# Optimization experiments

Hardware: AMD Instinct MI355X
Metric: run time of the kernel (lower is better)

Reference implementation:

```python
import jax, jax.numpy as jnp
import numpy as np

S, V, T = 128, 64, 128
N_RBF, CUTOFF = 16, 6.0
N_ATOM, N_PROT, N_FRAG, N_BATCH = 8192, 16384, 1024, 8
K, R, EPS = 32, 3.0, 1e-4
ES_DIM = N_RBF + S + S + T  # 400
HID = 256
GATE = S + 2 * V  # 256


def rbf_encode(d):
    mu = jnp.linspace(0.0, CUTOFF, N_RBF)
    gamma = N_RBF / CUTOFF
    return jnp.exp(-jnp.square(gamma * (d[..., None] - mu)))


def tp_conv(hs, hv, src, dst, diff, es, valid, n_dst, W1, b1, W2, b2, Ws, Wv):
    """Gather -> edge-scalar-gated tensor product -> scatter-add (EquivariantTPConv)."""
    w = jax.nn.silu(es @ W1 + b1) @ W2 + b2                      # [E, S+2V] edge gates
    unit = diff / (jnp.linalg.norm(diff, axis=-1, keepdims=True) + 1e-8)
    xs = hs[src] @ Ws                                            # [E, S]
    xv = jnp.einsum('evc,vw->ewc', hv[src], Wv)                  # [E, V, 3]
    ms = jnp.where(valid[:, None], w[:, :S] * xs, 0.0)
    mv = jnp.where(valid[:, None, None],
                   w[:, S:S + V, None] * xv + w[:, S + V:, None] * unit[:, None, :], 0.0)
    agg_s = jax.ops.segment_sum(ms, dst, num_segments=n_dst)
    agg_v = jax.ops.segment_sum(mv.reshape(-1, V * 3), dst, num_segments=n_dst).reshape(n_dst, V, 3)
    return agg_s, agg_v


def fragment_inertia(local_pos, fragment_id):
    r2 = jnp.sum(local_pos * local_pos, axis=-1)
    eye = jnp.eye(3, dtype=local_pos.dtype)
    I_atom = r2[:, None, None] * eye - local_pos[:, :, None] * local_pos[:, None, :]
    I_frag = jax.ops.segment_sum(I_atom.reshape(-1, 9), fragment_id, num_segments=N_FRAG).reshape(N_FRAG, 3, 3)
    trace = jnp.trace(I_frag, axis1=-2, axis2=-1)[:, None, None]
    return I_frag + EPS * jnp.maximum(trace, 1.0) * eye


def _forward(atom_pos, prot_pos, local_pos, h_atom_s, h_atom_v, h_prot_s, h_prot_v,
             h_frag_s, h_frag_v, t_emb_atom,
             W1_ra, b1_ra, W2_ra, b2_ra, Ws_ra, Wv_ra,
             W1_af, b1_af, W2_af, b2_af, Ws_af, Wv_af,
             Wo_s, Wo_v, Wf_s, Wf_v,
             fragment_id, atom_batch, prot_batch):
    # ---- bipartite radius graph prot -> atom via masked cdist + topk ----
    d2 = (jnp.sum(atom_pos * atom_pos, -1)[:, None]
          + jnp.sum(prot_pos * prot_pos, -1)[None, :]
          - 2.0 * atom_pos @ prot_pos.T)
    dist = jnp.sqrt(jnp.maximum(d2, 0.0))                        # [N_ATOM, N_PROT]
    mask = (dist <= R) & (atom_batch[:, None] == prot_batch[None, :])
    dinf = jnp.where(mask, dist, jnp.inf)
    neg_top, src = jax.lax.top_k(-dinf, K)                       # K nearest per atom
    valid = jnp.isfinite(neg_top).reshape(-1)
    src = src.reshape(-1)
    dst = jnp.repeat(jnp.arange(N_ATOM), K)
    # ---- residue->atom TP conv ----
    diff_ra = atom_pos[dst] - prot_pos[src]
    dist_ra = jnp.linalg.norm(diff_ra, axis=-1)
    ra_es = jnp.concatenate([rbf_encode(dist_ra), h_prot_s[src], h_atom_s[dst], t_emb_atom[dst]], -1)
    ms, mv = tp_conv(h_prot_s, h_prot_v, src, dst, diff_ra, ra_es, valid, N_ATOM,
                     W1_ra, b1_ra, W2_ra, b2_ra, Ws_ra, Wv_ra)
    ha_s = h_atom_s + jax.nn.silu(ms @ Wo_s)
    ha_v = h_atom_v + jnp.einsum('nvc,vw->nwc', mv, Wo_v)
    # ---- fragment centers + atom->frag re-lift TP conv ----
    ones = jnp.ones((N_ATOM,), atom_pos.dtype)
    cnt = jnp.maximum(jax.ops.segment_sum(ones, fragment_id, num_segments=N_FRAG), 1.0)
    T_frag = jax.ops.segment_sum(atom_pos, fragment_id, num_segments=N_FRAG) / cnt[:, None]
    r_af = atom_pos - T_frag[fragment_id]
    af_es = jnp.concatenate([rbf_encode(jnp.linalg.norm(r_af, axis=-1)), ha_s,
                             h_frag_s[fragment_id], t_emb_atom], -1)
    af_valid = jnp.ones((N_ATOM,), bool)
    fs, fv = tp_conv(ha_s, ha_v, jnp.arange(N_ATOM), fragment_id, r_af, af_es, af_valid, N_FRAG,
                     W1_af, b1_af, W2_af, b2_af, Ws_af, Wv_af)
    hf_s = h_frag_s + jax.nn.silu(fs @ Wf_s)
    hf_v = h_frag_v + jnp.einsum('nvc,vw->nwc', fv, Wf_v)
    I_frag = fragment_inertia(local_pos, fragment_id)
    # single packed output [N_ATOM, 2*(S+3V)+9]; frag quantities gathered per atom
    return jnp.concatenate([ha_s, ha_v.reshape(N_ATOM, -1),
                            hf_s[fragment_id], hf_v.reshape(N_FRAG, -1)[fragment_id],
                            I_frag.reshape(N_FRAG, 9)[fragment_id]], -1)


def setup_inputs() -> dict:
    key = jax.random.key(0)
    ks = jax.random.split(key, 32)
    def w(k, shape, fan_in):
        return jax.random.normal(k, shape, jnp.float32) / np.sqrt(fan_in).astype(np.float32)
    return dict(
        atom_pos=jax.random.normal(ks[0], (N_ATOM, 3), jnp.float32),
        prot_pos=jax.random.normal(ks[1], (N_PROT, 3), jnp.float32),
        local_pos=jax.random.normal(ks[2], (N_ATOM, 3), jnp.float32),
        h_atom_s=jax.random.normal(ks[3], (N_ATOM, S), jnp.float32),
        h_atom_v=jax.random.normal(ks[4], (N_ATOM, V, 3), jnp.float32),
        h_prot_s=jax.random.normal(ks[5], (N_PROT, S), jnp.float32),
        h_prot_v=jax.random.normal(ks[6], (N_PROT, V, 3), jnp.float32),
        h_frag_s=jax.random.normal(ks[7], (N_FRAG, S), jnp.float32),
        h_frag_v=jax.random.normal(ks[8], (N_FRAG, V, 3), jnp.float32),
        t_emb_atom=jax.random.normal(ks[9], (N_ATOM, T), jnp.float32),
        W1_ra=w(ks[10], (ES_DIM, HID), ES_DIM), b1_ra=jnp.zeros((HID,), jnp.float32),
        W2_ra=w(ks[11], (HID, GATE), HID), b2_ra=jnp.zeros((GATE,), jnp.float32),
        Ws_ra=w(ks[12], (S, S), S), Wv_ra=w(ks[13], (V, V), V),
        W1_af=w(ks[14], (ES_DIM, HID), ES_DIM), b1_af=jnp.zeros((HID,), jnp.float32),
        W2_af=w(ks[15], (HID, GATE), HID), b2_af=jnp.zeros((GATE,), jnp.float32),
        Ws_af=w(ks[16], (S, S), S), Wv_af=w(ks[17], (V, V), V),
        Wo_s=w(ks[18], (S, S), S), Wo_v=w(ks[19], (V, V), V),
        Wf_s=w(ks[20], (S, S), S), Wf_v=w(ks[21], (V, V), V),
        fragment_id=jax.random.randint(ks[22], (N_ATOM,), 0, N_FRAG),
        atom_batch=jnp.sort(jax.random.randint(ks[23], (N_ATOM,), 0, N_BATCH)),
        prot_batch=jnp.sort(jax.random.randint(ks[24], (N_PROT,), 0, N_BATCH)),
    )


def reference(atom_pos, prot_pos, local_pos, h_atom_s, h_atom_v, h_prot_s, h_prot_v,
              h_frag_s, h_frag_v, t_emb_atom,
              W1_ra, b1_ra, W2_ra, b2_ra, Ws_ra, Wv_ra,
              W1_af, b1_af, W2_af, b2_af, Ws_af, Wv_af,
              Wo_s, Wo_v, Wf_s, Wf_v,
              fragment_id, atom_batch, prot_batch):
    return _forward(atom_pos, prot_pos, local_pos, h_atom_s, h_atom_v, h_prot_s, h_prot_v,
                    h_frag_s, h_frag_v, t_emb_atom,
                    W1_ra, b1_ra, W2_ra, b2_ra, Ws_ra, Wv_ra,
                    W1_af, b1_af, W2_af, b2_af, Ws_af, Wv_af,
                    Wo_s, Wo_v, Wf_s, Wf_v,
                    fragment_id, atom_batch, prot_batch)
```

## Files before the change

kernel.cpp:

```cpp
#include <hip/hip_runtime.h>
#include <hip/hip_bf16.h>

#define N_ATOM 8192
#define N_PROT 16384
#define N_FRAG 1024
#define KNN    32
#define OUTC   649

typedef __attribute__((ext_vector_type(8))) short bf16x8;
typedef __attribute__((ext_vector_type(4))) float f32x4;

__device__ __forceinline__ float silu_f(float x){ return x / (1.f + __expf(-x)); }
__device__ __forceinline__ unsigned long long ullmin2(unsigned long long a, unsigned long long b){ return a < b ? a : b; }

__device__ __forceinline__ short f2bf(float x){
    __hip_bfloat16 h = __float2bfloat16(x);
    return *reinterpret_cast<short*>(&h);
}
__device__ __forceinline__ unsigned f2bf2(float lo, float hi){
    __hip_bfloat162 h2;
    h2.x = __float2bfloat16(lo);
    h2.y = __float2bfloat16(hi);
    return *reinterpret_cast<unsigned*>(&h2);
}
__device__ __forceinline__ float bf2f(short s){
    return __uint_as_float(((unsigned)(unsigned short)s) << 16);
}

__global__ void k_ranges(const int* __restrict__ pbatch, int* __restrict__ pstart){
    int b = threadIdx.x;
    if (b <= 8){
        int lo = 0, hi = N_PROT;
        while (lo < hi){ int mid = (lo + hi) >> 1; if (pbatch[mid] < b) lo = mid + 1; else hi = mid; }
        pstart[b] = lo;
    }
}

__global__ __launch_bounds__(256) void k_cvt(const float* __restrict__ hps,
                                             const float* __restrict__ hpv,
                                             short* __restrict__ hpsB,
                                             short* __restrict__ hpvT){
    int id = blockIdx.x*256 + threadIdx.x;
    if (id < N_PROT*16){
        const float* s = hps + (size_t)id*8;
        float4 x0 = *(const float4*)(s);
        float4 x1 = *(const float4*)(s+4);
        unsigned* d = (unsigned*)(hpsB + (size_t)id*8);
        d[0] = f2bf2(x0.x, x0.y); d[1] = f2bf2(x0.z, x0.w);
        d[2] = f2bf2(x1.x, x1.y); d[3] = f2bf2(x1.z, x1.w);
    } else {
        int id2 = id - N_PROT*16;
        if (id2 < N_PROT*24){
            int j = id2 / 24, r = id2 % 24;
            short tmp[8];
#pragma unroll
            for (int u = 0; u < 8; ++u){
                int o = r*8 + u, c = o >> 6, v = o & 63;
                tmp[u] = f2bf(hpv[(size_t)j*192 + v*3 + c]);
            }
            *(bf16x8*)(hpvT + (size_t)j*192 + r*8) = *(bf16x8*)tmp;
        }
    }
}

__global__ __launch_bounds__(256) void k_knn(const float* __restrict__ apos,
                                             const float* __restrict__ ppos,
                                             const int* __restrict__ abatch,
                                             const int* __restrict__ pstart,
                                             int* __restrict__ src_out){
    __shared__ int h1[256];
    __shared__ int s_info[4];
    __shared__ int s_nsel;
    __shared__ int s_nbound;
    __shared__ unsigned long long s_bound[512];

    const int i = blockIdx.x, t = threadIdx.x;
    const int lane = t & 63;
    const int b = abatch[i];
    const int p0 = pstart[b], p1 = pstart[b+1];
    const float ax = apos[i*3+0], ay = apos[i*3+1], az = apos[i*3+2];
    const float a2 = ax*ax + ay*ay + az*az;
    const float BINSCALE = 256.0f / 9.0f;

    unsigned kb[12];
    int jj[12];
    int bn[12];
#pragma unroll
    for (int q = 0; q < 12; ++q){
        int j = p0 + q*256 + t;
        unsigned kk = 0xFFFFFFFFu;
        int bin = -1;
        if (j < p1){
            float px = ppos[j*3+0], py = ppos[j*3+1], pz = ppos[j*3+2];
            float p2 = px*px + py*py + pz*pz;
            float dt = ax*px + ay*py + az*pz;
            float d2 = fmaxf((a2 + p2) - 2.0f*dt, 0.f);
            if (d2 <= 9.0f){
                kk = __float_as_uint(d2);
                bin = (int)(d2 * BINSCALE);
                if (bin > 255) bin = 255;
            }
        }
        kb[q] = kk; jj[q] = j; bn[q] = bin;
    }
    h1[t] = 0;
    if (t == 0){ s_nsel = 0; s_nbound = 0; }
    __syncthreads();
#pragma unroll
    for (int q = 0; q < 12; ++q)
        if (bn[q] >= 0) atomicAdd(&h1[bn[q]], 1);
    __syncthreads();
    if (t < 64){
        int base = t*4;
// ... 2 lines not shown
        int sc = lsum;
#pragma unroll
        for (int off = 1; off < 64; off <<= 1){
            int v = __shfl_up(sc, off);
            if (lane >= off) sc += v;
        }
        int ex = sc - lsum;
        h1[base]   = ex + a0;
        h1[base+1] = ex + a0 + a1;
        h1[base+2] = ex + a0 + a1 + a2i;
        h1[base+3] = sc;
        if (t == 63) s_info[3] = sc;
    }
    __syncthreads();
    const int total = s_info[3];
    const int kth = (total < KNN) ? total : KNN;
    if (kth > 0){
        int cum  = h1[t];
        int prev = (t == 0) ? 0 : h1[t-1];
        if (cum >= kth && prev < kth){ s_info[0] = t; }
    }
    __syncthreads();
    const int B = s_info[0];
    if (kth > 0){
#pragma unroll
        for (int q = 0; q < 12; ++q){
            if (bn[q] < 0) continue;
            if (bn[q] < B){
                int pos = atomicAdd(&s_nsel, 1);
                src_out[i*KNN + pos] = jj[q];
            } else if (bn[q] == B){
                int bi = atomicAdd(&s_nbound, 1);
                if (bi < 512) s_bound[bi] = ((unsigned long long)kb[q] << 32) | (unsigned)jj[q];
            }
        }
    }
    __syncthreads();
    const int base_n = s_nsel;
    const int R = kth - base_n;
    if (t < 64 && R > 0){
        int L = s_nbound; if (L > 512) L = 512;
        for (int r = 0; r < R; ++r){
            unsigned long long m = ~0ull;
            for (int idx = lane; idx < L; idx += 64) m = ullmin2(m, s_bound[idx]);
#pragma unroll
            for (int off = 32; off >= 1; off >>= 1)
                m = ullmin2(m, (unsigned long long)__shfl_xor((unsigned long long)m, off));
            if (lane == 0) src_out[i*KNN + base_n + r] = (int)(unsigned)(m & 0xFFFFFFFFull);
            for (int idx = lane; idx < L; idx += 64)
                if (s_bound[idx] == m) s_bound[idx] = ~0ull;
        }
    }
    if (t < KNN && t >= kth) src_out[i*KNN + t] = -1;
}

__global__ void k_fragsum(const float* __restrict__ apos, const float* __restrict__ lpos,
                          const int* __restrict__ fid,
                          float* __restrict__ cnt, float* __restrict__ tsum, float* __restrict__ isum){
    int a = blockIdx.x*256 + threadIdx.x;
    if (a >= N_ATOM) return;
    int f = fid[a];
    atomicAdd(&cnt[f], 1.f);
    atomicAdd(&tsum[f*3+0], apos[a*3+0]);
    atomicAdd(&tsum[f*3+1], apos[a*3+1]);
    atomicAdd(&tsum[f*3+2], apos[a*3+2]);
    float x = lpos[a*3+0], y = lpos[a*3+1], z = lpos[a*3+2];
    float r2 = x*x + y*y + z*z;
    atomicAdd(&isum[f*9+0], r2 - x*x);
    atomicAdd(&isum[f*9+1], -(x*y));
    atomicAdd(&isum[f*9+2], -(x*z));
    atomicAdd(&isum[f*9+3], -(y*x));
    atomicAdd(&isum[f*9+4], r2 - y*y);
    atomicAdd(&isum[f*9+5], -(y*z));
    atomicAdd(&isum[f*9+6], -(z*x));
    atomicAdd(&isum[f*9+7], -(z*y));
    atomicAdd(&isum[f*9+8], r2 - z*z);
}

__global__ __launch_bounds__(1024) void k_csr_prefix(const float* __restrict__ cnt,
                                                     const float* __restrict__ tsum,
                                                     const float* __restrict__ isum,
                                                     int* __restrict__ csr_off,
                                                     int* __restrict__ csr_cur,
                                                     float* __restrict__ tfrag,
                                                     float* __restrict__ ifin){
    __shared__ int s[1024];
    int t = threadIdx.x;
    float cn_raw = cnt[t];
    int v = (int)cn_raw;
    s[t] = v;
    {
        float cn = fmaxf(cn_raw, 1.f);
        tfrag[t*3+0] = tsum[t*3+0] / cn;
        tfrag[t*3+1] = tsum[t*3+1] / cn;
        tfrag[t*3+2] = tsum[t*3+2] / cn;
        float tr  = isum[t*9+0] + isum[t*9+4] + isum[t*9+8];
        float add = 1e-4f * fmaxf(tr, 1.f);
#pragma unroll
        for (int q = 0; q < 9; ++q){
            float vv = isum[t*9+q];
            if (q == 0 || q == 4 || q == 8) vv += add;
            ifin[t*9+q] = vv;
        }
    }
    __syncthreads();
    for (int off = 1; off < 1024; off <<= 1){
        int x = (t >= off) ? s[t-off] : 0;
        __syncthreads();
        s[t] += x;
        __syncthreads();
    }
    int incl = s[t];
    int excl = incl - v;
    csr_off[t] = excl;
    csr_cur[t] = excl;
    if (t == 1023) csr_off[1024] = incl;
}

__global__ void k_csr_scatter(const int* __restrict__ fid, int* __restrict__ csr_cur,
                              int* __restrict__ csr_atom){
    int a = blockIdx.x*256 + threadIdx.x;
    if (a >= N_ATOM) return;
    int f = fid[a];
    int pos = atomicAdd(&csr_cur[f], 1);
    csr_atom[pos] = a;
}

__global__ void k_pack(const float* __restrict__ W1, const float* __restrict__ W2,
                       const float* __restrict__ Ws, const float* __restrict__ Wv,
                       const float* __restrict__ W1a, const float* __restrict__ W2a,
                       const float* __restrict__ Wsa, const float* __restrict__ Wva,
                       const float* __restrict__ Wos, const float* __restrict__ Wov,
                       short* __restrict__ W1p, short* __restrict__ W2p,
                       short* __restrict__ Wsp, short* __restrict__ Wvp,
                       short* __restrict__ W1cp,
                       short* __restrict__ W1ap, short* __restrict__ W2ap,
                       short* __restrict__ Wsap, short* __restrict__ Wvap,
                       short* __restrict__ Wosp, short* __restrict__ Wovp){
    int id = blockIdx.x*256 + threadIdx.x;
    if (id < 5120){
        int kt = id/1024, rem = id%1024, nt = rem/64, l = rem%64;
#pragma unroll
        for (int jj = 0; jj < 8; ++jj){
            int k = kt*32 + ((l>>4)<<3) + jj, n = nt*16 + (l&15);
            W1p[(size_t)id*8 + jj] = (k < 144) ? f2bf(W1[(size_t)k*256 + n]) : (short)0;
        }
    } else if (id < 13312){
        int id2 = id - 5120;
        int kt = id2/1024, rem = id2%1024, nt = rem/64, l = rem%64;
#pragma unroll
        for (int jj = 0; jj < 8; ++jj){
            int k = kt*32 + ((l>>4)<<3) + jj, n = nt*16 + (l&15);
            W2p[(size_t)id2*8 + jj] = f2bf(W2[(size_t)k*256 + n]);
        }
    } else if (id < 15360){
        int id2 = id - 13312;
        int kt = id2/512, rem = id2%512, nt = rem/64, l = rem%64;
#pragma unroll
        for (int jj = 0; jj < 8; ++jj){
            int k = kt*32 + ((l>>4)<<3) + jj, n = nt*16 + (l&15);
            Wsp[(size_t)id2*8 + jj] = f2bf(Ws[(size_t)k*128 + n]);
        }
    } else if (id < 15872){
        int id2 = id - 15360;
        int kt = id2/256, rem = id2%256, nt = rem/64, l = rem%64;
#pragma unroll
        for (int jj = 0; jj < 8; ++jj){
            int k = kt*32 + ((l>>4)<<3) + jj, n = nt*16 + (l&15);
            Wvp[(size_t)id2*8 + jj] = f2bf(Wv[(size_t)k*64 + n]);
        }
    } else if (id < 24064){
        int id2 = id - 15872;
        int kt = id2/1024, rem = id2%1024, nt = rem/64, l = rem%64;
#pragma unroll
        for (int jj = 0; jj < 8; ++jj){
            int k = kt*32 + ((l>>4)<<3) + jj, n = nt*16 + (l&15);
            W1cp[(size_t)id2*8 + jj] = f2bf(W1[(size_t)(144 + k)*256 + n]);
        }
    } else if (id < 37376){
        int id2 = id - 24064;
        int kt = id2/1024, rem = id2%1024, nt = rem/64, l = rem%64;
#pragma unroll
        for (int jj = 0; jj < 8; ++jj){
            int k = kt*32 + ((l>>4)<<3) + jj, n = nt*16 + (l&15);
            W1ap[(size_t)id2*8 + jj] = (k < 400) ? f2bf(W1a[(size_t)k*256 + n]) : (short)0;
        }
    } else if (id < 45568){
        int id2 = id - 37376;
        int kt = id2/1024, rem = id2%1024, nt = rem/64, l = rem%64;
#pragma unroll
        for (int jj = 0; jj < 8; ++jj){
            int k = kt*32 + ((l>>4)<<3) + jj, n = nt*16 + (l&15);
            W2ap[(size_t)id2*8 + jj] = f2bf(W2a[(size_t)k*256 + n]);
        }
    } else if (id < 47616){
        int id2 = id - 45568;
        int kt = id2/512, rem = id2%512, nt = rem/64, l = rem%64;
#pragma unroll
        for (int jj = 0; jj < 8; ++jj){
            int k = kt*32 + ((l>>4)<<3) + jj, n = nt*16 + (l&15);
            Wsap[(size_t)id2*8 + jj] = f2bf(Wsa[(size_t)k*128 + n]);
        }
    } else if (id < 48128){
        int id2 = id - 47616;
        int kt = id2/256, rem = id2%256, nt = rem/64, l = rem%64;
#pragma unroll
        for (int jj = 0; jj < 8; ++jj){
            int k = kt*32 + ((l>>4)<<3) + jj, n = nt*16 + (l&15);
            Wvap[(size_t)id2*8 + jj] = f2bf(Wva[(size_t)k*64 + n]);
        }
    } else if (id < 50176){
        int id2 = id - 48128;
        int kt = id2/512, rem = id2%512, nt = rem/64, l = rem%64;
#pragma unroll
        for (int jj = 0; jj < 8; ++jj){
            int k = kt*32 + ((l>>4)<<3) + jj, n = nt*16 + (l&15);
            Wosp[(size_t)id2*8 + jj] = f2bf(Wos[(size_t)k*128 + n]);
        }
    } else if (id < 50688){
        int id2 = id - 50176;
        int kt = id2/256, rem = id2%256, nt = rem/64, l = rem%64;
#pragma unroll
        for (int jj = 0; jj < 8; ++jj){
            int k = kt*32 + ((l>>4)<<3) + jj, n = nt*16 + (l&15);
            Wovp[(size_t)id2*8 + jj] = f2bf(Wov[(size_t)k*64 + n]);
        }
    }
}

__global__ __launch_bounds__(256) void k_ctx(const float* __restrict__ has_,
                                             const float* __restrict__ temb,
                                             const short* __restrict__ W1cp,
                                             const float* __restrict__ b1,
                                             float* __restrict__ common){
    __shared__ __align__(16) char s_a[64*512];
    const int t = threadIdx.x, l = t & 63, w = t >> 6, g = l >> 4;
    const int a0 = blockIdx.x * 64;
    {
        int r = t & 63, seg = t >> 6;
        const float* srcp = (seg < 2) ? (has_ + (size_t)(a0 + r)*128 + seg*64)
                                      : (temb + (size_t)(a0 + r)*128 + (seg - 2)*64);
#pragma unroll
        for (int q = 0; q < 16; ++q){
            float4 x = *(const float4*)(srcp + q*4);
            int col = seg*64 + q*4;
            int off = (r*512 + col*2) ^ ((r & 7) << 4);
            *(unsigned*)(s_a + off)     = f2bf2(x.x, x.y);
            *(unsigned*)(s_a + off + 4) = f2bf2(x.z, x.w);
        }
    }
    __syncthreads();
    f32x4 acc[4][4];
#pragma unroll
    for (int mt = 0; mt < 4; ++mt)
#pragma unroll
        for (int nt = 0; nt < 4; ++nt) acc[mt][nt] = (f32x4){0.f,0.f,0.f,0.f};
    for (int ks = 0; ks < 8; ++ks){
        bf16x8 afr[4];
#pragma unroll
        for (int mt = 0; mt < 4; ++mt){
            int row = mt*16 + (l & 15);
            int off = (row*512 + ks*64 + g*16) ^ ((row & 7) << 4);
            afr[mt] = *(const bf16x8*)(s_a + off);
        }
#pragma unroll
        for (int nt = 0; nt < 4; ++nt){
            bf16x8 b = *(const bf16x8*)(W1cp + ((size_t)((ks*16 + (w*4 + nt))*64 + l))*8);
#pragma unroll
            for (int mt = 0; mt < 4; ++mt)
                acc[mt][nt] = __builtin_amdgcn_mfma_f32_16x16x32_bf16(afr[mt], b, acc[mt][nt], 0, 0, 0);
        }
    }
#pragma unroll
    for (int nt = 0; nt < 4; ++nt){
        int col = w*64 + nt*16 + (l & 15);
        float bb = b1[col];
#pragma unroll
        for (int mt = 0; mt < 4; ++mt)
#pragma unroll
            for (int r = 0; r < 4; ++r){
                int row = mt*16 + g*4 + r;
                common[(size_t)(a0 + row)*256 + col] = acc[mt][nt][r] + bb;
// ... 178 lines not shown
                }
            }
#pragma unroll
            for (int nt = 0; nt < 2; ++nt){
                float p = 0.f;
#pragma unroll
                for (int mt = 0; mt < 2; ++mt)
#pragma unroll
                    for (int r = 0; r < 4; ++r)
                        p = fmaf(accw[mt][nt][r] + b2v[nt], accxv[mt][nt][r], p);
                p += __shfl_xor(p, 16);
                p += __shfl_xor(p, 32);
                if (l < 16) s_mvA[c*64 + (w-4)*32 + nt*16 + r0] = p;
            }
        }
    } else {
        float uu[8][3];
#pragma unroll
        for (int mt = 0; mt < 2; ++mt)
#pragma unroll
            for (int r = 0; r < 4; ++r){
                int e = mt*16 + g*4 + r;
#pragma unroll
                for (int c = 0; c < 3; ++c) uu[mt*4+r][c] = s_unit[e][c];
            }
#pragma unroll
        for (int c = 0; c < 3; ++c)
#pragma unroll
            for (int nt = 0; nt < 2; ++nt){
                float p = 0.f;
#pragma unroll
                for (int mt = 0; mt < 2; ++mt)
#pragma unroll
                    for (int r = 0; r < 4; ++r)
                        p = fmaf(accw[mt][nt][r] + b2v[nt], uu[mt*4+r][c], p);
                p += __shfl_xor(p, 16);
                p += __shfl_xor(p, 32);
                if (l < 16) s_mvB[c*64 + (w-6)*32 + nt*16 + r0] = p;
            }
    }
    __syncthreads();

    if (t < 192){
        int wi = t & 63, cc = t >> 6;
        float v = s_mvA[cc*64 + wi] + s_mvB[cc*64 + wi];
        mvR[((size_t)i*3 + cc)*64 + wi] = f2bf(v);
    }
}

__global__ __launch_bounds__(256) void k_ra_out(
    const short* __restrict__ msR, const short* __restrict__ mvR,
    const short* __restrict__ Wosp, const short* __restrict__ Wovp,
    const float* __restrict__ has_, const float* __restrict__ hav,
    float* __restrict__ out)
{
    const int t = threadIdx.x, l = t & 63, w = t >> 6, g = l >> 4, r0 = l & 15;
    const int a0 = blockIdx.x * 32;

    f32x4 acc[2][2];
#pragma unroll
    for (int mt = 0; mt < 2; ++mt)
#pragma unroll
        for (int nt = 0; nt < 2; ++nt) acc[mt][nt] = (f32x4){0.f,0.f,0.f,0.f};
    for (int ks = 0; ks < 4; ++ks){
        bf16x8 af0 = *(const bf16x8*)(msR + ((size_t)(a0 + r0)*128 + ks*32 + g*8));
        bf16x8 af1 = *(const bf16x8*)(msR + ((size_t)(a0 + 16 + r0)*128 + ks*32 + g*8));
#pragma unroll
        for (int nt = 0; nt < 2; ++nt){
            bf16x8 b = *(const bf16x8*)(Wosp + ((size_t)((ks*8 + (w*2 + nt))*64 + l))*8);
            acc[0][nt] = __builtin_amdgcn_mfma_f32_16x16x32_bf16(af0, b, acc[0][nt], 0, 0, 0);
            acc[1][nt] = __builtin_amdgcn_mfma_f32_16x16x32_bf16(af1, b, acc[1][nt], 0, 0, 0);
        }
    }
#pragma unroll
    for (int nt = 0; nt < 2; ++nt){
        int col = w*32 + nt*16 + r0;
#pragma unroll
        for (int mt = 0; mt < 2; ++mt)
#pragma unroll
            for (int r = 0; r < 4; ++r){
                int a = a0 + mt*16 + g*4 + r;
                out[(size_t)a*OUTC + col] = has_[(size_t)a*128 + col] + silu_f(acc[mt][nt][r]);
            }
    }

    f32x4 accv[6];
#pragma unroll
    for (int mt = 0; mt < 6; ++mt) accv[mt] = (f32x4){0.f,0.f,0.f,0.f};
    for (int ks = 0; ks < 2; ++ks){
        bf16x8 b = *(const bf16x8*)(Wovp + ((size_t)((ks*4 + w)*64 + l))*8);
#pragma unroll
        for (int mt = 0; mt < 6; ++mt){
            bf16x8 af = *(const bf16x8*)(mvR + ((size_t)(a0*3 + mt*16 + r0)*64 + ks*32 + g*8));
            accv[mt] = __builtin_amdgcn_mfma_f32_16x16x32_bf16(af, b, accv[mt], 0, 0, 0);
        }
    }
    const int wi = w*16 + r0;
#pragma unroll
    for (int mt = 0; mt < 6; ++mt)
#pragma unroll
        for (int r = 0; r < 4; ++r){
            int R = mt*16 + g*4 + r;
            int a = a0 + R/3, c = R - (R/3)*3;
            out[(size_t)a*OUTC + 128 + wi*3 + c] = hav[(size_t)a*192 + wi*3 + c] + accv[mt][r];
        }
}

#define AES_STR 848
__global__ __launch_bounds__(256, 2) void k_af2(
    const float* __restrict__ apos, const float* __restrict__ tfrag,
    const float* __restrict__ hfs_in, const float* __restrict__ temb,
    const short* __restrict__ W1p, const float* __restrict__ b1,
    const short* __restrict__ W2p, const float* __restrict__ b2,
    const short* __restrict__ Wsp, const short* __restrict__ Wvp,
    const int* __restrict__ fragid, const float* __restrict__ out,
    short* __restrict__ msA, short* __restrict__ mvA)
{
    __shared__ __align__(16) char s_es[16*AES_STR];
    __shared__ __align__(16) char s_h1[16*512];
    __shared__ __align__(16) char s_pv[3*2048];
    __shared__ float s_unit[16][3];
    float* s_upr = (float*)s_es;

    const int t = threadIdx.x, a0 = blockIdx.x*16;
    const int l = t & 63, w = t >> 6, g = l >> 4, r0 = l & 15;
    const int xm = (r0 & 7) << 4;

    {
        const int e = t >> 4, sub = t & 15;
        const int a = a0 + e;
        const int f = fragid[a];
        float rx = apos[a*3+0] - tfrag[f*3+0];
        float ry = apos[a*3+1] - tfrag[f*3+1];
        float rz = apos[a*3+2] - tfrag[f*3+2];
        float dist = sqrtf(rx*rx + ry*ry + rz*rz);
        if (sub == 0){
            float inv = 1.f / (dist + 1e-8f);
            s_unit[e][0] = rx*inv; s_unit[e][1] = ry*inv; s_unit[e][2] = rz*inv;
        }
        if (sub < 2){
            const float gamma = 16.0f / 6.0f;
#pragma unroll
            for (int q = 0; q < 4; ++q){
                int kk = sub*8 + q*2;
                float mu0  = 0.4f * (float)kk;
                float mu1  = 0.4f * (float)(kk+1);
                float a0f = gamma * (dist - mu0);
                float a1f = gamma * (dist - mu1);
                *(unsigned*)(s_es + e*AES_STR + kk*2) = f2bf2(__expf(-(a0f*a0f)), __expf(-(a1f*a1f)));
            }
        }
#pragma unroll
        for (int q = 0; q < 4; ++q){
            float v0 = out[(size_t)a*OUTC + sub*8 + q*2];
            float v1 = out[(size_t)a*OUTC + sub*8 + q*2 + 1];
            *(unsigned*)(s_es + e*AES_STR + 32 + (sub*8 + q*2)*2) = f2bf2(v0, v1);
        }
#pragma unroll
        for (int q = 0; q < 2; ++q){
            float4 x = *(const float4*)(hfs_in + (size_t)f*128 + sub*8 + q*4);
            *(unsigned*)(s_es + e*AES_STR + 288 + sub*16 + q*8)     = f2bf2(x.x, x.y);
            *(unsigned*)(s_es + e*AES_STR + 288 + sub*16 + q*8 + 4) = f2bf2(x.z, x.w);
        }
#pragma unroll
        for (int q = 0; q < 2; ++q){
            float4 x = *(const float4*)(temb + (size_t)a*128 + sub*8 + q*4);
            *(unsigned*)(s_es + e*AES_STR + 544 + sub*16 + q*8)     = f2bf2(x.x, x.y);
            *(unsigned*)(s_es + e*AES_STR + 544 + sub*16 + q*8 + 4) = f2bf2(x.z, x.w);
        }
        *(short*)(s_es + e*AES_STR + 800 + sub*2) = 0;
        const int em = (e & 7) << 4;
#pragma unroll
        for (int q = 0; q < 12; ++q){
            int idx = sub*12 + q;
            float v = out[(size_t)a*OUTC + 128 + idx];
            int vv = idx/3, c = idx - vv*3;
            *(short*)(s_pv + c*2048 + e*128 + ((vv*2) ^ em)) = f2bf(v);
        }
    }
    __syncthreads();

    f32x4 acc1[4];
#pragma unroll
    for (int nt = 0; nt < 4; ++nt) acc1[nt] = (f32x4){0.f,0.f,0.f,0.f};
    for (int ks = 0; ks < 13; ++ks){
        bf16x8 a0f = *(const bf16x8*)(s_es + r0*AES_STR + ks*64 + g*16);
#pragma unroll
        for (int nt = 0; nt < 4; ++nt){
            bf16x8 b = *(const bf16x8*)(W1p + ((size_t)((ks*16 + (w*4 + nt))*64 + l))*8);
            acc1[nt] = __builtin_amdgcn_mfma_f32_16x16x32_bf16(a0f, b, acc1[nt], 0, 0, 0);
        }
    }
#pragma unroll
    for (int nt = 0; nt < 4; ++nt){
        int col = w*64 + nt*16 + r0;
        float bb = b1[col];
#pragma unroll
        for (int r = 0; r < 4; ++r){
            float v = silu_f(acc1[nt][r] + bb);
            int row = g*4 + r;
            int off = (row*512 + col*2) ^ ((row & 7) << 4);
            *(short*)(s_h1 + off) = f2bf(v);
        }
    }
    f32x4 accxs[4];
#pragma unroll
    for (int nt = 0; nt < 4; ++nt) accxs[nt] = (f32x4){0.f,0.f,0.f,0.f};
    if (w < 2){
        for (int ks = 0; ks < 4; ++ks){
            bf16x8 a0f = *(const bf16x8*)(s_es + r0*AES_STR + 32 + ks*64 + g*16);
#pragma unroll
            for (int nt = 0; nt < 4; ++nt){
                bf16x8 b = *(const bf16x8*)(Wsp + ((size_t)((ks*8 + (w*4 + nt))*64 + l))*8);
                accxs[nt] = __builtin_amdgcn_mfma_f32_16x16x32_bf16(a0f, b, accxs[nt], 0, 0, 0);
            }
        }
    }
    __syncthreads();

    f32x4 accw[4];
#pragma unroll
    for (int nt = 0; nt < 4; ++nt) accw[nt] = (f32x4){0.f,0.f,0.f,0.f};
    for (int ks = 0; ks < 8; ++ks){
        int off0 = (r0*512 + ks*64 + g*16) ^ xm;
        bf16x8 a0f = *(const bf16x8*)(s_h1 + off0);
#pragma unroll
        for (int nt = 0; nt < 4; ++nt){
            bf16x8 b = *(const bf16x8*)(W2p + ((size_t)((ks*16 + (w*4 + nt))*64 + l))*8);
            accw[nt] = __builtin_amdgcn_mfma_f32_16x16x32_bf16(a0f, b, accw[nt], 0, 0, 0);
        }
// ... 128 lines not shown
        }
        float val = hfv_in[f*192 + wi*3 + cc] + o;
        for (int n = n0; n < n1; ++n)
            out[(size_t)csr_atom[n]*OUTC + 448 + wi*3 + cc] = val;
    } else if (t < 201){
        int q = t - 192;
        float val = ifin[f*9 + q];
        for (int n = n0; n < n1; ++n)
            out[(size_t)csr_atom[n]*OUTC + 640 + q] = val;
    }
}

extern "C" void kernel_launch(void* const* d_in, const int* in_sizes, int n_in,
                              void* d_out, int out_size, void* d_ws, size_t ws_size,
                              hipStream_t stream)
{
    const float* atom_pos   = (const float*)d_in[0];
    const float* prot_pos   = (const float*)d_in[1];
    const float* local_pos  = (const float*)d_in[2];
    const float* h_atom_s   = (const float*)d_in[3];
    const float* h_atom_v   = (const float*)d_in[4];
    const float* h_prot_s   = (const float*)d_in[5];
    const float* h_prot_v   = (const float*)d_in[6];
    const float* h_frag_s   = (const float*)d_in[7];
    const float* h_frag_v   = (const float*)d_in[8];
    const float* t_emb      = (const float*)d_in[9];
    const float* W1_ra = (const float*)d_in[10]; const float* b1_ra = (const float*)d_in[11];
    const float* W2_ra = (const float*)d_in[12]; const float* b2_ra = (const float*)d_in[13];
    const float* Ws_ra = (const float*)d_in[14]; const float* Wv_ra = (const float*)d_in[15];
    const float* W1_af = (const float*)d_in[16]; const float* b1_af = (const float*)d_in[17];
    const float* W2_af = (const float*)d_in[18]; const float* b2_af = (const float*)d_in[19];
    const float* Ws_af = (const float*)d_in[20]; const float* Wv_af = (const float*)d_in[21];
    const float* Wo_s  = (const float*)d_in[22]; const float* Wo_v  = (const float*)d_in[23];
    const float* Wf_s  = (const float*)d_in[24]; const float* Wf_v  = (const float*)d_in[25];
    const int* fragment_id = (const int*)d_in[26];
    const int* atom_batch  = (const int*)d_in[27];
    const int* prot_batch  = (const int*)d_in[28];
    float* out = (float*)d_out;

    float* cnt   = (float*)d_ws;
    float* tsum  = cnt  + 1024;
    float* isum  = tsum + 3072;
    float* tfrag = isum + 9216;
    float* ifin  = tfrag + 3072;
    float* hfs   = ifin + 9216;
    float* hfv   = hfs  + 1024*128;
    int*   pstart   = (int*)(hfv + 1024*192);
    int*   src      = pstart + 16;
    int*   csr_off  = src + N_ATOM*KNN;
    int*   csr_cur  = csr_off + 1025;
    int*   csr_atom = csr_cur + 1024;
    uintptr_t pal = ((uintptr_t)(csr_atom + 8192) + 127) & ~(uintptr_t)127;
    float* common = (float*)pal;
    short* msA = (short*)common;
    short* mvA = msA + (size_t)8192*128;
    short* W1p  = (short*)(common + (size_t)8192*256);
    short* W2p  = W1p  + 40960;
    short* Wsp  = W2p  + 65536;
    short* Wvp  = Wsp  + 16384;
    short* W1cp = Wvp  + 4096;
    short* W1ap = W1cp + 65536;
    short* W2ap = W1ap + 106496;
    short* Wsap = W2ap + 65536;
    short* Wvap = Wsap + 16384;
    short* Wosp = Wvap + 4096;
    short* Wovp = Wosp + 16384;
    short* msR  = Wovp + 4096;
    short* mvR  = msR + (size_t)8192*128;
    short* hpsB = mvR + (size_t)8192*192;
    short* hpvT = hpsB + (size_t)N_PROT*128;

    size_t zero_bytes = (size_t)(1024 + 3072 + 9216) * sizeof(float);
    hipMemsetAsync(cnt, 0, zero_bytes, stream);

    k_pack    <<<198, 256, 0, stream>>>(W1_ra, W2_ra, Ws_ra, Wv_ra, W1_af, W2_af, Ws_af, Wv_af,
                                        Wo_s, Wo_v,
                                        W1p, W2p, Wsp, Wvp, W1cp, W1ap, W2ap, Wsap, Wvap,
                                        Wosp, Wovp);
    k_cvt     <<<(N_PROT*16 + N_PROT*24)/256, 256, 0, stream>>>(h_prot_s, h_prot_v, hpsB, hpvT);
    k_ranges  <<<1, 64, 0, stream>>>(prot_batch, pstart);
    k_knn     <<<N_ATOM, 256, 0, stream>>>(atom_pos, prot_pos, atom_batch, pstart, src);
    k_ctx     <<<N_ATOM/64, 256, 0, stream>>>(h_atom_s, t_emb, W1cp, b1_ra, common);
    k_fragsum <<<N_ATOM/256, 256, 0, stream>>>(atom_pos, local_pos, fragment_id, cnt, tsum, isum);
    k_csr_prefix<<<1, 1024, 0, stream>>>(cnt, tsum, isum, csr_off, csr_cur, tfrag, ifin);
    k_csr_scatter<<<N_ATOM/256, 256, 0, stream>>>(fragment_id, csr_cur, csr_atom);
    k_ra3     <<<N_ATOM, 512, 0, stream>>>(atom_pos, prot_pos, hpsB, hpvT,
                                           W1p, W2p, Wsp, Wvp, common, b2_ra,
                                           src, msR, mvR);
    k_ra_out  <<<N_ATOM/32, 256, 0, stream>>>(msR, mvR, Wosp, Wovp, h_atom_s, h_atom_v, out);
    k_af2     <<<N_ATOM/16, 256, 0, stream>>>(atom_pos, tfrag, h_frag_s, t_emb,
                                              W1ap, b1_af, W2ap, b2_af, Wsap, Wvap,
                                              fragment_id, out, msA, mvA);
    k_fragupd <<<N_FRAG, 256, 0, stream>>>(csr_off, csr_atom, msA, mvA,
                                           h_frag_s, h_frag_v, Wf_s, Wf_v, ifin, out);
}
```

Baseline: 244.1 us.

## Merge prep kernels and hand bf16 atom features to the fragment stage

Folds weight packing, protein feature conversion, batch range search, fragment sums and new bf16 conversions of fragment scalars and time embeddings into one prep kernel. This cuts several small kernel launches. The RA output kernel also writes bf16 copies of the updated atom scalars and a channel-transposed bf16 copy of the atom vectors. The AF kernel then loads these with wide 16-byte loads instead of strided fp32 reads from the output plus per-element conversion. The cost is extra workspace and extra stores in k_ra_out.

Result: faster. 232.1 us (-4.9%).

```diff
diff --git a/kernel.cpp b/kernel.cpp
--- a/kernel.cpp
+++ b/kernel.cpp
@@ -27,38 +27,200 @@
     return __uint_as_float(((unsigned)(unsigned short)s) << 16);
 }
 
-__global__ void k_ranges(const int* __restrict__ pbatch, int* __restrict__ pstart){
-    int b = threadIdx.x;
-    if (b <= 8){
-        int lo = 0, hi = N_PROT;
-        while (lo < hi){ int mid = (lo + hi) >> 1; if (pbatch[mid] < b) lo = mid + 1; else hi = mid; }
-        pstart[b] = lo;
-    }
-}
-
-__global__ __launch_bounds__(256) void k_cvt(const float* __restrict__ hps,
-                                             const float* __restrict__ hpv,
-                                             short* __restrict__ hpsB,
-                                             short* __restrict__ hpvT){
-    int id = blockIdx.x*256 + threadIdx.x;
-    if (id < N_PROT*16){
-        const float* s = hps + (size_t)id*8;
+__device__ void dev_pack(int id,
+                         const float* __restrict__ W1, const float* __restrict__ W2,
+                         const float* __restrict__ Ws, const float* __restrict__ Wv,
+                         const float* __restrict__ W1a, const float* __restrict__ W2a,
+                         const float* __restrict__ Wsa, const float* __restrict__ Wva,
+                         const float* __restrict__ Wos, const float* __restrict__ Wov,
+                         short* __restrict__ W1p, short* __restrict__ W2p,
+                         short* __restrict__ Wsp, short* __restrict__ Wvp,
+                         short* __restrict__ W1cp,
+                         short* __restrict__ W1ap, short* __restrict__ W2ap,
+                         short* __restrict__ Wsap, short* __restrict__ Wvap,
+                         short* __restrict__ Wosp, short* __restrict__ Wovp){
+    if (id < 5120){
+        int kt = id/1024, rem = id%1024, nt = rem/64, l = rem%64;
+#pragma unroll
+        for (int jj = 0; jj < 8; ++jj){
+            int k = kt*32 + ((l>>4)<<3) + jj, n = nt*16 + (l&15);
+            W1p[(size_t)id*8 + jj] = (k < 144) ? f2bf(W1[(size_t)k*256 + n]) : (short)0;
+        }
+    } else if (id < 13312){
+        int id2 = id - 5120;
+        int kt = id2/1024, rem = id2%1024, nt = rem/64, l = rem%64;
+#pragma unroll
+        for (int jj = 0; jj < 8; ++jj){
+            int k = kt*32 + ((l>>4)<<3) + jj, n = nt*16 + (l&15);
+            W2p[(size_t)id2*8 + jj] = f2bf(W2[(size_t)k*256 + n]);
+        }
+    } else if (id < 15360){
+        int id2 = id - 13312;
+        int kt = id2/512, rem = id2%512, nt = rem/64, l = rem%64;
+#pragma unroll
+        for (int jj = 0; jj < 8; ++jj){
+            int k = kt*32 + ((l>>4)<<3) + jj, n = nt*16 + (l&15);
+            Wsp[(size_t)id2*8 + jj] = f2bf(Ws[(size_t)k*128 + n]);
+        }
+    } else if (id < 15872){
+        int id2 = id - 15360;
+        int kt = id2/256, rem = id2%256, nt = rem/64, l = rem%64;
+#pragma unroll
+        for (int jj = 0; jj < 8; ++jj){
+            int k = kt*32 + ((l>>4)<<3) + jj, n = nt*16 + (l&15);
+            Wvp[(size_t)id2*8 + jj] = f2bf(Wv[(size_t)k*64 + n]);
+        }
+    } else if (id < 24064){
+        int id2 = id - 15872;
+        int kt = id2/1024, rem = id2%1024, nt = rem/64, l = rem%64;
+#pragma unroll
+        for (int jj = 0; jj < 8; ++jj){
+            int k = kt*32 + ((l>>4)<<3) + jj, n = nt*16 + (l&15);
+            W1cp[(size_t)id2*8 + jj] = f2bf(W1[(size_t)(144 + k)*256 + n]);
+        }
+    } else if (id < 37376){
+        int id2 = id - 24064;
+        int kt = id2/1024, rem = id2%1024, nt = rem/64, l = rem%64;
+#pragma unroll
+        for (int jj = 0; jj < 8; ++jj){
+            int k = kt*32 + ((l>>4)<<3) + jj, n = nt*16 + (l&15);
+            W1ap[(size_t)id2*8 + jj] = (k < 400) ? f2bf(W1a[(size_t)k*256 + n]) : (short)0;
+        }
+    } else if (id < 45568){
+        int id2 = id - 37376;
+        int kt = id2/1024, rem = id2%1024, nt = rem/64, l = rem%64;
+#pragma unroll
+        for (int jj = 0; jj < 8; ++jj){
+            int k = kt*32 + ((l>>4)<<3) + jj, n = nt*16 + (l&15);
+            W2ap[(size_t)id2*8 + jj] = f2bf(W2a[(size_t)k*256 + n]);
+        }
+    } else if (id < 47616){
+        int id2 = id - 45568;
+        int kt = id2/512, rem = id2%512, nt = rem/64, l = rem%64;
+#pragma unroll
+        for (int jj = 0; jj < 8; ++jj){
+            int k = kt*32 + ((l>>4)<<3) + jj, n = nt*16 + (l&15);
+            Wsap[(size_t)id2*8 + jj] = f2bf(Wsa[(size_t)k*128 + n]);
+        }
+    } else if (id < 48128){
+        int id2 = id - 47616;
+        int kt = id2/256, rem = id2%256, nt = rem/64, l = rem%64;
+#pragma unroll
+        for (int jj = 0; jj < 8; ++jj){
+            int k = kt*32 + ((l>>4)<<3) + jj, n = nt*16 + (l&15);
+            Wvap[(size_t)id2*8 + jj] = f2bf(Wva[(size_t)k*64 + n]);
+        }
+    } else if (id < 50176){
+        int id2 = id - 48128;
+        int kt = id2/512, rem = id2%512, nt = rem/64, l = rem%64;
+#pragma unroll
+        for (int jj = 0; jj < 8; ++jj){
+            int k = kt*32 + ((l>>4)<<3) + jj, n = nt*16 + (l&15);
+            Wosp[(size_t)id2*8 + jj] = f2bf(Wos[(size_t)k*128 + n]);
+        }
+    } else if (id < 50688){
+        int id2 = id - 50176;
+        int kt = id2/256, rem = id2%256, nt = rem/64, l = rem%64;
+#pragma unroll
+        for (int jj = 0; jj < 8; ++jj){
+            int k = kt*32 + ((l>>4)<<3) + jj, n = nt*16 + (l&15);
+            Wovp[(size_t)id2*8 + jj] = f2bf(Wov[(size_t)k*64 + n]);
+        }
+    }
+}
+
+#define PREP_B0 198
+#define PREP_B1 (PREP_B0 + 2560)
+#define PREP_B2 (PREP_B1 + 1)
+#define PREP_B3 (PREP_B2 + 64)
+#define PREP_B4 (PREP_B3 + 512)
+#define PREP_NB (PREP_B4 + 32)
+__global__ __launch_bounds__(256) void k_prep(
+    const float* __restrict__ W1, const float* __restrict__ W2,
+    const float* __restrict__ Ws, const float* __restrict__ Wv,
+    const float* __restrict__ W1a, const float* __restrict__ W2a,
+    const float* __restrict__ Wsa, const float* __restrict__ Wva,
+    const float* __restrict__ Wos, const float* __restrict__ Wov,
+    const float* __restrict__ hps, const float* __restrict__ hpv,
+    const float* __restrict__ hfsF, const float* __restrict__ tembF,
+    const float* __restrict__ apos, const float* __restrict__ lpos,
+    const int* __restrict__ fid, const int* __restrict__ pbatch,
+    short* __restrict__ W1p, short* __restrict__ W2p,
+    short* __restrict__ Wsp, short* __restrict__ Wvp,
+    short* __restrict__ W1cp,
+    short* __restrict__ W1ap, short* __restrict__ W2ap,
+    short* __restrict__ Wsap, short* __restrict__ Wvap,
+    short* __restrict__ Wosp, short* __restrict__ Wovp,
+    short* __restrict__ hpsB, short* __restrict__ hpvT,
+    short* __restrict__ hfsB, short* __restrict__ tembB,
+    int* __restrict__ pstart,
+    float* __restrict__ cnt, float* __restrict__ tsum, float* __restrict__ isum)
+{
+    const int b = blockIdx.x, t = threadIdx.x;
+    if (b < PREP_B0){
+        dev_pack(b*256 + t, W1, W2, Ws, Wv, W1a, W2a, Wsa, Wva, Wos, Wov,
+                 W1p, W2p, Wsp, Wvp, W1cp, W1ap, W2ap, Wsap, Wvap, Wosp, Wovp);
+    } else if (b < PREP_B1){
+        int id = (b - PREP_B0)*256 + t;
+        if (id < N_PROT*16){
+            const float* s = hps + (size_t)id*8;
+            float4 x0 = *(const float4*)(s);
+            float4 x1 = *(const float4*)(s+4);
+            unsigned* d = (unsigned*)(hpsB + (size_t)id*8);
+            d[0] = f2bf2(x0.x, x0.y); d[1] = f2bf2(x0.z, x0.w);
+            d[2] = f2bf2(x1.x, x1.y); d[3] = f2bf2(x1.z, x1.w);
+        } else {
+            int id2 = id - N_PROT*16;
+            int j = id2 / 24, r = id2 % 24;
+            short tmp[8];
+#pragma unroll
+            for (int u = 0; u < 8; ++u){
+                int o = r*8 + u, c = o >> 6, v = o & 63;
+                tmp[u] = f2bf(hpv[(size_t)j*192 + v*3 + c]);
+            }
+            *(bf16x8*)(hpvT + (size_t)j*192 + r*8) = *(bf16x8*)tmp;
+        }
+    } else if (b < PREP_B2){
+        if (t <= 8){
+            int lo = 0, hi = N_PROT;
+            while (lo < hi){ int mid = (lo + hi) >> 1; if (pbatch[mid] < t) lo = mid + 1; else hi = mid; }
+            pstart[t] = lo;
+        }
+    } else if (b < PREP_B3){
+        int id = (b - PREP_B2)*256 + t;
+        const float* s = hfsF + (size_t)id*8;
         float4 x0 = *(const float4*)(s);
         float4 x1 = *(const float4*)(s+4);
-        unsigned* d = (unsigned*)(hpsB + (size_t)id*8);
+        unsigned* d = (unsigned*)(hfsB + (size_t)id*8);
+        d[0] = f2bf2(x0.x, x0.y); d[1] = f2bf2(x0.z, x0.w);
+        d[2] = f2bf2(x1.x, x1.y); d[3] = f2bf2(x1.z, x1.w);
+    } else if (b < PREP_B4){
+        int id = (b - PREP_B3)*256 + t;
+        const float* s = tembF + (size_t)id*8;
+        float4 x0 = *(const float4*)(s);
+        float4 x1 = *(const float4*)(s+4);
+        unsigned* d = (unsigned*)(tembB + (size_t)id*8);
         d[0] = f2bf2(x0.x, x0.y); d[1] = f2bf2(x0.z, x0.w);
         d[2] = f2bf2(x1.x, x1.y); d[3] = f2bf2(x1.z, x1.w);
     } else {
-        int id2 = id - N_PROT*16;
-        if (id2 < N_PROT*24){
-            int j = id2 / 24, r = id2 % 24;
-            short tmp[8];
-#pragma unroll
-            for (int u = 0; u < 8; ++u){
-                int o = r*8 + u, c = o >> 6, v = o & 63;
-                tmp[u] = f2bf(hpv[(size_t)j*192 + v*3 + c]);
-            }
-            *(bf16x8*)(hpvT + (size_t)j*192 + r*8) = *(bf16x8*)tmp;
+        int a = (b - PREP_B4)*256 + t;
+        if (a < N_ATOM){
+            int f = fid[a];
+            atomicAdd(&cnt[f], 1.f);
+            atomicAdd(&tsum[f*3+0], apos[a*3+0]);
+            atomicAdd(&tsum[f*3+1], apos[a*3+1]);
+            atomicAdd(&tsum[f*3+2], apos[a*3+2]);
+            float x = lpos[a*3+0], y = lpos[a*3+1], z = lpos[a*3+2];
+            float r2 = x*x + y*y + z*z;
+            atomicAdd(&isum[f*9+0], r2 - x*x);
+            atomicAdd(&isum[f*9+1], -(x*y));
+            atomicAdd(&isum[f*9+2], -(x*z));
+            atomicAdd(&isum[f*9+3], -(y*x));
+            atomicAdd(&isum[f*9+4], r2 - y*y);
+            atomicAdd(&isum[f*9+5], -(y*z));
+            atomicAdd(&isum[f*9+6], -(z*x));
+            atomicAdd(&isum[f*9+7], -(z*y));
+            atomicAdd(&isum[f*9+8], r2 - z*z);
         }
     }
 }
@@ -167,29 +329,6 @@
         }
     }
     if (t < KNN && t >= kth) src_out[i*KNN + t] = -1;
-}
-
-__global__ void k_fragsum(const float* __restrict__ apos, const float* __restrict__ lpos,
-                          const int* __restrict__ fid,
-                          float* __restrict__ cnt, float* __restrict__ tsum, float* __restrict__ isum){
-    int a = blockIdx.x*256 + threadIdx.x;
-    if (a >= N_ATOM) return;
-    int f = fid[a];
-    atomicAdd(&cnt[f], 1.f);
-    atomicAdd(&tsum[f*3+0], apos[a*3+0]);
-    atomicAdd(&tsum[f*3+1], apos[a*3+1]);
-    atomicAdd(&tsum[f*3+2], apos[a*3+2]);
-    float x = lpos[a*3+0], y = lpos[a*3+1], z = lpos[a*3+2];
-    float r2 = x*x + y*y + z*z;
-    atomicAdd(&isum[f*9+0], r2 - x*x);
-    atomicAdd(&isum[f*9+1], -(x*y));
-    atomicAdd(&isum[f*9+2], -(x*z));
-    atomicAdd(&isum[f*9+3], -(y*x));
-    atomicAdd(&isum[f*9+4], r2 - y*y);
-    atomicAdd(&isum[f*9+5], -(y*z));
-    atomicAdd(&isum[f*9+6], -(z*x));
-    atomicAdd(&isum[f*9+7], -(z*y));
-    atomicAdd(&isum[f*9+8], r2 - z*z);
 }
 
 __global__ __launch_bounds__(1024) void k_csr_prefix(const float* __restrict__ cnt,
@@ -241,108 +380,6 @@
     csr_atom[pos] = a;
 }
 
-__global__ void k_pack(const float* __restrict__ W1, const float* __restrict__ W2,
-                       const float* __restrict__ Ws, const float* __restrict__ Wv,
-                       const float* __restrict__ W1a, const float* __restrict__ W2a,
-                       const float* __restrict__ Wsa, const float* __restrict__ Wva,
-                       const float* __restrict__ Wos, const float* __restrict__ Wov,
-                       short* __restrict__ W1p, short* __restrict__ W2p,
-                       short* __restrict__ Wsp, short* __restrict__ Wvp,
-                       short* __restrict__ W1cp,
-                       short* __restrict__ W1ap, short* __restrict__ W2ap,
-                       short* __restrict__ Wsap, short* __restrict__ Wvap,
-                       short* __restrict__ Wosp, short* __restrict__ Wovp){
-    int id = blockIdx.x*256 + threadIdx.x;
-    if (id < 5120){
-        int kt = id/1024, rem = id%1024, nt = rem/64, l = rem%64;
-#pragma unroll
-        for (int jj = 0; jj < 8; ++jj){
-            int k = kt*32 + ((l>>4)<<3) + jj, n = nt*16 + (l&15);
-            W1p[(size_t)id*8 + jj] = (k < 144) ? f2bf(W1[(size_t)k*256 + n]) : (short)0;
-        }
-    } else if (id < 13312){
-        int id2 = id - 5120;
-        int kt = id2/1024, rem = id2%1024, nt = rem/64, l = rem%64;
-#pragma unroll
-        for (int jj = 0; jj < 8; ++jj){
-            int k = kt*32 + ((l>>4)<<3) + jj, n = nt*16 + (l&15);
-            W2p[(size_t)id2*8 + jj] = f2bf(W2[(size_t)k*256 + n]);
-        }
-    } else if (id < 15360){
-        int id2 = id - 13312;
-        int kt = id2/512, rem = id2%512, nt = rem/64, l = rem%64;
-#pragma unroll
-        for (int jj = 0; jj < 8; ++jj){
-            int k = kt*32 + ((l>>4)<<3) + jj, n = nt*16 + (l&15);
-            Wsp[(size_t)id2*8 + jj] = f2bf(Ws[(size_t)k*128 + n]);
-        }
-    } else if (id < 15872){
-        int id2 = id - 15360;
-        int kt = id2/256, rem = id2%256, nt = rem/64, l = rem%64;
-#pragma unroll
-        for (int jj = 0; jj < 8; ++jj){
-            int k = kt*32 + ((l>>4)<<3) + jj, n = nt*16 + (l&15);
-            Wvp[(size_t)id2*8 + jj] = f2bf(Wv[(size_t)k*64 + n]);
-        }
-    } else if (id < 24064){
-        int id2 = id - 15872;
-        int kt = id2/1024, rem = id2%1024, nt = rem/64, l = rem%64;
-#pragma unroll
-        for (int jj = 0; jj < 8; ++jj){
-            int k = kt*32 + ((l>>4)<<3) + jj, n = nt*16 + (l&15);
-            W1cp[(size_t)id2*8 + jj] = f2bf(W1[(size_t)(144 + k)*256 + n]);
-        }
-    } else if (id < 37376){
-        int id2 = id - 24064;
-        int kt = id2/1024, rem = id2%1024, nt = rem/64, l = rem%64;
-#pragma unroll
-        for (int jj = 0; jj < 8; ++jj){
-            int k = kt*32 + ((l>>4)<<3) + jj, n = nt*16 + (l&15);
-            W1ap[(size_t)id2*8 + jj] = (k < 400) ? f2bf(W1a[(size_t)k*256 + n]) : (short)0;
-        }
-    } else if (id < 45568){
-        int id2 = id - 37376;
-        int kt = id2/1024, rem = id2%1024, nt = rem/64, l = rem%64;
-#pragma unroll
-        for (int jj = 0; jj < 8; ++jj){
-            int k = kt*32 + ((l>>4)<<3) + jj, n = nt*16 + (l&15);
-            W2ap[(size_t)id2*8 + jj] = f2bf(W2a[(size_t)k*256 + n]);
-        }
-    } else if (id < 47616){
-        int id2 = id - 45568;
-        int kt = id2/512, rem = id2%512, nt = rem/64, l = rem%64;
-#pragma unroll
-        for (int jj = 0; jj < 8; ++jj){
-            int k = kt*32 + ((l>>4)<<3) + jj, n = nt*16 + (l&15);
-            Wsap[(size_t)id2*8 + jj] = f2bf(Wsa[(size_t)k*128 + n]);
-        }
-    } else if (id < 48128){
-        int id2 = id - 47616;
-        int kt = id2/256, rem = id2%256, nt = rem/64, l = rem%64;
-#pragma unroll
-        for (int jj = 0; jj < 8; ++jj){
-            int k = kt*32 + ((l>>4)<<3) + jj, n = nt*16 + (l&15);
-            Wvap[(size_t)id2*8 + jj] = f2bf(Wva[(size_t)k*64 + n]);
-        }
-    } else if (id < 50176){
-        int id2 = id - 48128;
-        int kt = id2/512, rem = id2%512, nt = rem/64, l = rem%64;
-#pragma unroll
-        for (int jj = 0; jj < 8; ++jj){
-            int k = kt*32 + ((l>>4)<<3) + jj, n = nt*16 + (l&15);
-            Wosp[(size_t)id2*8 + jj] = f2bf(Wos[(size_t)k*128 + n]);
-        }
-    } else if (id < 50688){
-        int id2 = id - 50176;
-        int kt = id2/256, rem = id2%256, nt = rem/64, l = rem%64;
-#pragma unroll
-        for (int jj = 0; jj < 8; ++jj){
-            int k = kt*32 + ((l>>4)<<3) + jj, n = nt*16 + (l&15);
-            Wovp[(size_t)id2*8 + jj] = f2bf(Wov[(size_t)k*64 + n]);
-        }
-    }
-}
-
 __global__ __launch_bounds__(256) void k_ctx(const float* __restrict__ has_,
                                              const float* __restrict__ temb,
                                              const short* __restrict__ W1cp,
@@ -627,7 +664,8 @@
     const short* __restrict__ msR, const short* __restrict__ mvR,
     const short* __restrict__ Wosp, const short* __restrict__ Wovp,
     const float* __restrict__ has_, const float* __restrict__ hav,
-    float* __restrict__ out)
+    float* __restrict__ out,
+    short* __restrict__ haB, short* __restrict__ havT)
 {
     const int t = threadIdx.x, l = t & 63, w = t >> 6, g = l >> 4, r0 = l & 15;
     const int a0 = blockIdx.x * 32;
@@ -655,7 +693,9 @@
 #pragma unroll
             for (int r = 0; r < 4; ++r){
                 int a = a0 + mt*16 + g*4 + r;
-                out[(size_t)a*OUTC + col] = has_[(size_t)a*128 + col] + silu_f(acc[mt][nt][r]);
+                float val = has_[(size_t)a*128 + col] + silu_f(acc[mt][nt][r]);
+                out[(size_t)a*OUTC + col] = val;
+                haB[(size_t)a*128 + col] = f2bf(val);
             }
     }
 
@@ -677,18 +717,21 @@
         for (int r = 0; r < 4; ++r){
             int R = mt*16 + g*4 + r;
             int a = a0 + R/3, c = R - (R/3)*3;
-            out[(size_t)a*OUTC + 128 + wi*3 + c] = hav[(size_t)a*192 + wi*3 + c] + accv[mt][r];
+            float val = hav[(size_t)a*192 + wi*3 + c] + accv[mt][r];
+            out[(size_t)a*OUTC + 128 + wi*3 + c] = val;
+            havT[(size_t)a*192 + c*64 + wi] = f2bf(val);
         }
 }
 
 #define AES_STR 848
 __global__ __launch_bounds__(256, 2) void k_af2(
     const float* __restrict__ apos, const float* __restrict__ tfrag,
-    const float* __restrict__ hfs_in, const float* __restrict__ temb,
+    const short* __restrict__ haB, const short* __restrict__ hfsB,
+    const short* __restrict__ tembB, const short* __restrict__ havT,
     const short* __restrict__ W1p, const float* __restrict__ b1,
     const short* __restrict__ W2p, const float* __restrict__ b2,
     const short* __restrict__ Wsp, const short* __restrict__ Wvp,
-    const int* __restrict__ fragid, const float* __restrict__ out,
+    const int* __restrict__ fragid,
     short* __restrict__ msA, short* __restrict__ mvA)
 {
     __shared__ __align__(16) char s_es[16*AES_STR];
@@ -725,32 +768,18 @@
                 *(unsigned*)(s_es + e*AES_STR + kk*2) = f2bf2(__expf(-(a0f*a0f)), __expf(-(a1f*a1f)));
             }
         }
-#pragma unroll
-        for (int q = 0; q < 4; ++q){
-            float v0 = out[(size_t)a*OUTC + sub*8 + q*2];
-            float v1 = out[(size_t)a*OUTC + sub*8 + q*2 + 1];
-            *(unsigned*)(s_es + e*AES_STR + 32 + (sub*8 + q*2)*2) = f2bf2(v0, v1);
-        }
-#pragma unroll
-        for (int q = 0; q < 2; ++q){
-            float4 x = *(const float4*)(hfs_in + (size_t)f*128 + sub*8 + q*4);
-            *(unsigned*)(s_es + e*AES_STR + 288 + sub*16 + q*8)     = f2bf2(x.x, x.y);
-            *(unsigned*)(s_es + e*AES_STR + 288 + sub*16 + q*8 + 4) = f2bf2(x.z, x.w);
-        }
-#pragma unroll
-        for (int q = 0; q < 2; ++q){
-            float4 x = *(const float4*)(temb + (size_t)a*128 + sub*8 + q*4);
-            *(unsigned*)(s_es + e*AES_STR + 544 + sub*16 + q*8)     = f2bf2(x.x, x.y);
-            *(unsigned*)(s_es + e*AES_STR + 544 + sub*16 + q*8 + 4) = f2bf2(x.z, x.w);
-        }
+        *(bf16x8*)(s_es + e*AES_STR + 32  + sub*16) = *(const bf16x8*)(haB  + (size_t)a*128 + sub*8);
+        *(bf16x8*)(s_es + e*AES_STR + 288 + sub*16) = *(const bf16x8*)(hfsB + (size_t)f*128 + sub*8);
+        *(bf16x8*)(s_es + e*AES_STR + 544 + sub*16) = *(const bf16x8*)(tembB + (size_t)a*128 + sub*8);
         *(short*)(s_es + e*AES_STR + 800 + sub*2) = 0;
         const int em = (e & 7) << 4;
-#pragma unroll
-        for (int q = 0; q < 12; ++q){
-            int idx = sub*12 + q;
-            float v = out[(size_t)a*OUTC + 128 + idx];
-            int vv = idx/3, c = idx - vv*3;
-            *(short*)(s_pv + c*2048 + e*128 + ((vv*2) ^ em)) = f2bf(v);
+        {
+            bf16x8 c0 = *(const bf16x8*)(havT + (size_t)a*192 + sub*8);
+            *(bf16x8*)(s_pv + (sub>>3)*2048 + e*128 + (((sub&7)<<4) ^ em)) = c0;
+            if (sub < 8){
+                bf16x8 c1 = *(const bf16x8*)(havT + (size_t)a*192 + (16+sub)*8);
+                *(bf16x8*)(s_pv + 2*2048 + e*128 + ((sub<<4) ^ em)) = c1;
+            }
         }
     }
     __syncthreads();
@@ -985,8 +1014,9 @@
     int*   csr_atom = csr_cur + 1024;
     uintptr_t pal = ((uintptr_t)(csr_atom + 8192) + 127) & ~(uintptr_t)127;
     float* common = (float*)pal;
-    short* msA = (short*)common;
-    short* mvA = msA + (size_t)8192*128;
+    short* msA  = (short*)common;
+    short* mvA  = msA + (size_t)8192*128;
+    short* havT = mvA + (size_t)8192*192;
     short* W1p  = (short*)(common + (size_t)8192*256);
     short* W2p  = W1p  + 40960;
     short* Wsp  = W2p  + 65536;
@@ -1002,28 +1032,33 @@
     short* mvR  = msR + (size_t)8192*128;
     short* hpsB = mvR + (size_t)8192*192;
     short* hpvT = hpsB + (size_t)N_PROT*128;
+    short* haB  = hpvT + (size_t)N_PROT*192;
+    short* hfsB = haB + (size_t)8192*128;
+    short* tembB= hfsB + (size_t)1024*128;
 
     size_t zero_bytes = (size_t)(1024 + 3072 + 9216) * sizeof(float);
     hipMemsetAsync(cnt, 0, zero_bytes, stream);
 
-    k_pack    <<<198, 256, 0, stream>>>(W1_ra, W2_ra, Ws_ra, Wv_ra, W1_af, W2_af, Ws_af, Wv_af,
-                                        Wo_s, Wo_v,
-                                        W1p, W2p, Wsp, Wvp, W1cp, W1ap, W2ap, Wsap, Wvap,
-                                        Wosp, Wovp);
-    k_cvt     <<<(N_PROT*16 + N_PROT*24)/256, 256, 0, stream>>>(h_prot_s, h_prot_v, hpsB, hpvT);
-    k_ranges  <<<1, 64, 0, stream>>>(prot_batch, pstart);
+    k_prep    <<<PREP_NB, 256, 0, stream>>>(W1_ra, W2_ra, Ws_ra, Wv_ra, W1_af, W2_af, Ws_af, Wv_af,
+                                            Wo_s, Wo_v,
+                                            h_prot_s, h_prot_v, h_frag_s, t_emb,
+                                            atom_pos, local_pos, fragment_id, prot_batch,
+                                            W1p, W2p, Wsp, Wvp, W1cp, W1ap, W2ap, Wsap, Wvap,
+                                            Wosp, Wovp,
+                                            hpsB, hpvT, hfsB, tembB, pstart,
+                                            cnt, tsum, isum);
     k_knn     <<<N_ATOM, 256, 0, stream>>>(atom_pos, prot_pos, atom_batch, pstart, src);
     k_ctx     <<<N_ATOM/64, 256, 0, stream>>>(h_atom_s, t_emb, W1cp, b1_ra, common);
-    k_fragsum <<<N_ATOM/256, 256, 0, stream>>>(atom_pos, local_pos, fragment_id, cnt, tsum, isum);
     k_csr_prefix<<<1, 1024, 0, stream>>>(cnt, tsum, isum, csr_off, csr_cur, tfrag, ifin);
     k_csr_scatter<<<N_ATOM/256, 256, 0, stream>>>(fragment_id, csr_cur, csr_atom);
     k_ra3     <<<N_ATOM, 512, 0, stream>>>(atom_pos, prot_pos, hpsB, hpvT,
                                            W1p, W2p, Wsp, Wvp, common, b2_ra,
                                            src, msR, mvR);
-    k_ra_out  <<<N_ATOM/32, 256, 0, stream>>>(msR, mvR, Wosp, Wovp, h_atom_s, h_atom_v, out);
-    k_af2     <<<N_ATOM/16, 256, 0, stream>>>(atom_pos, tfrag, h_frag_s, t_emb,
+    k_ra_out  <<<N_ATOM/32, 256, 0, stream>>>(msR, mvR, Wosp, Wovp, h_atom_s, h_atom_v, out,
+                                              haB, havT);
+    k_af2     <<<N_ATOM/16, 256, 0, stream>>>(atom_pos, tfrag, haB, hfsB, tembB, havT,
                                               W1ap, b1_af, W2ap, b2_af, Wsap, Wvap,
-                                              fragment_id, out, msA, mvA);
+                                              fragment_id, msA, mvA);
     k_fragupd <<<N_FRAG, 256, 0, stream>>>(csr_off, csr_atom, msA, mvA,
                                            h_frag_s, h_frag_v, Wf_s, Wf_v, ifin, out);
 }
```
